# Optimization experiments

Measured on AMD Instinct MI355X. Metric: run time of the kernel, lower is better.

Reference implementation:

```python
import jax, jax.numpy as jnp
import numpy as np

N_REC = 12288  # 12 * nside^2, nside=32


def _mlp(x, w1, b1, w2, b2):
    # two-layer MLP with SiLU, as in GraphCast-style edge embedders
    return jnp.dot(jax.nn.silu(jnp.dot(x, w1) + b1), w2) + b2


def setup_inputs() -> dict:
    key = jax.random.key(0)
    ks = jax.random.split(key, 12)
    B, E, D_X, D_EDGE = 2, 393216, 128, 4
    EDGE_IN, EDGE_OUT, LIN_OUT = D_EDGE + D_X, 256, 256

    def glorot(k, shape):
        fan = shape[0] + shape[1]
        return jax.random.normal(k, shape, jnp.float32) * jnp.sqrt(2.0 / fan)

    return {
        "x": jax.random.normal(ks[0], (B, E, D_X), jnp.float32),
        "edge_attr": jax.random.normal(ks[1], (E, D_EDGE), jnp.float32),
        "edge_index": jax.random.randint(ks[2], (2, E), 0, N_REC, jnp.int64),
        "w1e": glorot(ks[3], (EDGE_IN, EDGE_OUT)),
        "b1e": jnp.zeros((EDGE_OUT,), jnp.float32),
        "w2e": glorot(ks[4], (EDGE_OUT, EDGE_OUT)),
        "b2e": jnp.zeros((EDGE_OUT,), jnp.float32),
        "w1f": glorot(ks[5], (EDGE_OUT, LIN_OUT)),
        "b1f": jnp.zeros((LIN_OUT,), jnp.float32),
        "w2f": glorot(ks[6], (LIN_OUT, LIN_OUT)),
        "b2f": jnp.zeros((LIN_OUT,), jnp.float32),
    }


def reference(x, edge_attr, edge_index, w1e, b1e, w2e, b2e, w1f, b1f, w2f, b2f):
    B = x.shape[0]
    # broadcast edge_attr over batch and concat with per-edge grid features
    ea = jnp.broadcast_to(edge_attr[None], (B,) + edge_attr.shape)  # [B,E,d_edge]
    v_g_prime = jnp.concatenate([ea, x], axis=-1)                    # [B,E,edge_in]
    v_g = _mlp(v_g_prime, w1e, b1e, w2e, b2e)                        # [B,E,edge_out]
    # scatter-sum edges into receiver nodes (edge_index[1]) along dim 1
    recv = edge_index[1]
    v_m_sum = jnp.zeros((B, N_REC, v_g.shape[-1]), v_g.dtype).at[:, recv].add(v_g)
    return _mlp(v_m_sum, w1f, b1f, w2f, b2f)                         # [B,N_REC,lin_out]
```

## Files before the change

### kernel.cpp

```cpp
#include <hip/hip_runtime.h>
#include <hip/hip_bf16.h>

#define E_EDGES 393216
#define NRECV   12288
#define DX      128
#define BATCH   2

typedef short bf16x8 __attribute__((ext_vector_type(8)));
typedef float f32x4  __attribute__((ext_vector_type(4)));

__device__ __forceinline__ unsigned short f2bf(float f) {
  union { float f; unsigned u; } v; v.f = f;
  unsigned r = v.u + 0x7FFFu + ((v.u >> 16) & 1u);
  return (unsigned short)(r >> 16);
}

__device__ __forceinline__ unsigned pk2(float a, float b) {
  __hip_bfloat162 h = __float22bfloat162_rn(make_float2(a, b));
  union { __hip_bfloat162 h; unsigned u; } c; c.h = h;
  return c.u;
}

__device__ __forceinline__ float silu_f(float v) {
  float e = __builtin_amdgcn_exp2f(v * -1.44269504089f);
  return v * __builtin_amdgcn_rcpf(1.0f + e);
}

__global__ __launch_bounds__(256) void zero_kernel(float4* __restrict__ p, int n4) {
  int i = blockIdx.x * 256 + threadIdx.x;
  int stride = gridDim.x * 256;
  float4 z = make_float4(0.f, 0.f, 0.f, 0.f);
  for (; i < n4; i += stride) p[i] = z;
}

__global__ __launch_bounds__(256) void swz_all_kernel(
    const float* __restrict__ w1e, const float* __restrict__ b1e,
    const float* __restrict__ w2e, const float* __restrict__ w1f,
    const float* __restrict__ w2f,
    unsigned short* __restrict__ w1sw, unsigned short* __restrict__ w2esw,
    unsigned short* __restrict__ w1fsw, unsigned short* __restrict__ w2fsw) {
  int blk = blockIdx.x;
  if (blk < 160) {
    int t = blk * 256 + threadIdx.x;
    int j = t & 7, l = (t >> 3) & 63, rest = t >> 9;
    int nf = rest & 15, ks = rest >> 4;
    int k = ks * 32 + (l >> 4) * 8 + j;
    int n = nf * 16 + (l & 15);
    float v = (k < 132) ? w1e[k * 256 + n] : (k == 132 ? b1e[n] : 0.0f);
    w1sw[t] = f2bf(v);
  } else {
    int g = blk - 160;
    int which = g >> 8;
    int t = (g & 255) * 256 + threadIdx.x;
    const float* W = (which == 0) ? w2e : (which == 1) ? w1f : w2f;
    unsigned short* O = (which == 0) ? w2esw : (which == 1) ? w1fsw : w2fsw;
    int j = t & 7, l = (t >> 3) & 63, rest = t >> 9;
    int nf = rest & 15, ks = rest >> 4;
    int k = ks * 32 + (l >> 4) * 8 + j;
    int n = nf * 16 + (l & 15);
    O[t] = f2bf(W[k * 256 + n]);
  }
}

__global__ void hist_kernel(const int* __restrict__ recv, int* __restrict__ cnt) {
  int e = blockIdx.x * 256 + threadIdx.x;
  if (e < E_EDGES) atomicAdd(&cnt[recv[e]], 1);
}

__global__ __launch_bounds__(256) void scan_kernel(const int* __restrict__ cnt,
                                                   int* __restrict__ head) {
  __shared__ int ts[256];
  const int t = threadIdx.x;
  const int base = t * 48;
  int s = 0;
#pragma unroll
  for (int i = 0; i < 48; ++i) s += cnt[base + i];
  ts[t] = s;
  __syncthreads();
  for (int d = 1; d < 256; d <<= 1) {
    int v = (t >= d) ? ts[t - d] : 0;
    __syncthreads();
    ts[t] += v;
    __syncthreads();
  }
  int run = (t == 0) ? 0 : ts[t - 1];
  for (int i = 0; i < 48; ++i) { head[base + i] = run; run += cnt[base + i]; }
}

__global__ void scatter_kernel(const int* __restrict__ recv, int* __restrict__ head,
                               int* __restrict__ perm) {
  int e = blockIdx.x * 256 + threadIdx.x;
  if (e < E_EDGES) {
    int pos = atomicAdd(&head[recv[e]], 1);
    perm[pos] = e;
  }
}

__global__ __launch_bounds__(256, 4) void edge_kernel(
    const float* __restrict__ x, const float* __restrict__ edge_attr,
    const int* __restrict__ recv, const int* __restrict__ perm,
    const unsigned short* __restrict__ w1sw, float* __restrict__ s) {
  __shared__ __align__(16) char As[64 * 384];
  __shared__ int rs[64];
  __shared__ int seg_recv[64];
  __shared__ unsigned seg32[16];

  const int tid = threadIdx.x;
  const int l  = tid & 63;
  const int w  = tid >> 6;
  const int lo = l & 15, hi = l >> 4;
  const int p0 = blockIdx.x * 64;
  const int b  = blockIdx.y;

  const int r = tid >> 2, q = tid & 3;
  const int er = perm[p0 + r];
  const float4* xr = (const float4*)(x + ((size_t)b * E_EDGES + er) * DX);
  float4 xv[8];
#pragma unroll
  for (int i = 0; i < 8; ++i) xv[i] = xr[i * 4 + q];

  float4 ea;
  if (tid < 64) {
    int e1 = perm[p0 + tid];
    rs[tid] = recv[e1];
    ea = *(const float4*)(edge_attr + (size_t)e1 * 4);
  }

  for (int idx = tid; idx < 960; idx += 256) {
    int rr = idx / 15, k2 = idx - rr * 15;
    int byte0 = 264 + 8 * k2;
    uint2 vz = make_uint2(k2 == 0 ? 0x00003F80u : 0u, 0u);
    *(uint2*)(As + rr * 384 + (byte0 ^ ((rr & 7) << 4))) = vz;
  }

  {
    const int rx = (r & 7) << 4;
#pragma unroll
    for (int i = 0; i < 8; ++i) {
      int t = i * 4 + q;
      int byte0 = 8 + 8 * t;
      *(uint2*)(As + r * 384 + (byte0 ^ rx)) =
          make_uint2(pk2(xv[i].x, xv[i].y), pk2(xv[i].z, xv[i].w));
    }
  }
  if (tid < 64) {
    *(uint2*)(As + tid * 384 + ((tid & 7) << 4)) =
        make_uint2(pk2(ea.x, ea.y), pk2(ea.z, ea.w));
  }
  __syncthreads();

  const int flag = (l == 63) || (rs[l + 1] != rs[l]);
  const unsigned long long segmask = __ballot(flag);
  const int nseg = __popcll(segmask);
  if (tid < 64) {
    int sid = __popcll(segmask & ((1ull << tid) - 1ull));
    ((unsigned char*)seg32)[tid] = (unsigned char)sid;
    if (flag) seg_recv[sid] = rs[tid];
  }

  f32x4 acc[4][4] = {};
  const int axor = (lo & 7) << 4;
  const unsigned short* wbase = w1sw + ((size_t)(w * 4) * 64 + l) * 8;
  bf16x8 cur0 = *(const bf16x8*)(wbase + 0 * 512);
  bf16x8 cur1 = *(const bf16x8*)(wbase + 1 * 512);
  bf16x8 cur2 = *(const bf16x8*)(wbase + 2 * 512);
  bf16x8 cur3 = *(const bf16x8*)(wbase + 3 * 512);
#pragma unroll
  for (int kk = 0; kk < 5; ++kk) {
    bf16x8 a[4];
#pragma unroll
    for (int mf = 0; mf < 4; ++mf)
      a[mf] = *(const bf16x8*)(As + (mf * 16 + lo) * 384 + ((kk * 64 + hi * 16) ^ axor));
    bf16x8 nxt0, nxt1, nxt2, nxt3;
    if (kk < 4) {
      const unsigned short* wn = wbase + (size_t)(kk + 1) * 8192;
      nxt0 = *(const bf16x8*)(wn + 0 * 512);
      nxt1 = *(const bf16x8*)(wn + 1 * 512);
      nxt2 = *(const bf16x8*)(wn + 2 * 512);
      nxt3 = *(const bf16x8*)(wn + 3 * 512);
    }
    __builtin_amdgcn_s_setprio(1);
#pragma unroll
    for (int mf = 0; mf < 4; ++mf)
      acc[mf][0] = __builtin_amdgcn_mfma_f32_16x16x32_bf16(a[mf], cur0, acc[mf][0], 0, 0, 0);
#pragma unroll
    for (int mf = 0; mf < 4; ++mf)
      acc[mf][1] = __builtin_amdgcn_mfma_f32_16x16x32_bf16(a[mf], cur1, acc[mf][1], 0, 0, 0);
#pragma unroll
    for (int mf = 0; mf < 4; ++mf)
      acc[mf][2] = __builtin_amdgcn_mfma_f32_16x16x32_bf16(a[mf], cur2, acc[mf][2], 0, 0, 0);
#pragma unroll
    for (int mf = 0; mf < 4; ++mf)
      acc[mf][3] = __builtin_amdgcn_mfma_f32_16x16x32_bf16(a[mf], cur3, acc[mf][3], 0, 0, 0);
    __builtin_amdgcn_s_setprio(0);
    if (kk < 4) { cur0 = nxt0; cur1 = nxt1; cur2 = nxt2; cur3 = nxt3; }
  }
  __syncthreads();

  unsigned pkd[4][4][2];
#pragma unroll
  for (int mf = 0; mf < 4; ++mf)
#pragma unroll
    for (int nf = 0; nf < 4; ++nf) {
      float v0 = silu_f(acc[mf][nf][0]);
      float v1 = silu_f(acc[mf][nf][1]);
      float v2 = silu_f(acc[mf][nf][2]);
      float v3 = silu_f(acc[mf][nf][3]);
      pkd[mf][nf][0] = pk2(v0, v1);
      pkd[mf][nf][1] = pk2(v2, v3);
    }

  unsigned hbw[2][4][4];
#pragma unroll
  for (int kk = 0; kk < 2; ++kk)
#pragma unroll
    for (int nf = 0; nf < 4; ++nf)
#pragma unroll
      for (int t = 0; t < 4; ++t) {
        int src = ((hi & 1) * 2 + (t >> 1)) * 16 + lo;
        int a0 = __shfl((int)pkd[2 * kk][nf][t & 1], src, 64);
        int a1 = __shfl((int)pkd[2 * kk + 1][nf][t & 1], src, 64);
        hbw[kk][nf][t] = (hi & 2) ? (unsigned)a1 : (unsigned)a0;
      }

  float* sb = s + (size_t)b * NRECV * 256;
  for (int p = 0; p * 16 < nseg; ++p) {
    union { unsigned u[4]; bf16x8 v; } ia[2];
#pragma unroll
    for (int kk = 0; kk < 2; ++kk) {
      unsigned d0 = seg32[kk * 8 + hi * 2];
      unsigned d1 = seg32[kk * 8 + hi * 2 + 1];
      unsigned tgt = (unsigned)(lo + p * 16);
      ia[kk].u[0] = (((d0 & 255u) == tgt) ? 0x3F80u : 0u) |
                    ((((d0 >> 8) & 255u) == tgt) ? 0x3F800000u : 0u);
      ia[kk].u[1] = ((((d0 >> 16) & 255u) == tgt) ? 0x3F80u : 0u) |
                    (((d0 >> 24) == tgt) ? 0x3F800000u : 0u);
      ia[kk].u[2] = (((d1 & 255u) == tgt) ? 0x3F80u : 0u) |
                    ((((d1 >> 8) & 255u) == tgt) ? 0x3F800000u : 0u);
      ia[kk].u[3] = ((((d1 >> 16) & 255u) == tgt) ? 0x3F80u : 0u) |
                    (((d1 >> 24) == tgt) ? 0x3F800000u : 0u);
    }
    f32x4 accS[4] = {};
    __builtin_amdgcn_s_setprio(1);
#pragma unroll
    for (int kk = 0; kk < 2; ++kk)
#pragma unroll
      for (int nf = 0; nf < 4; ++nf) {
        union { unsigned u[4]; bf16x8 v; } hb;
        hb.u[0] = hbw[kk][nf][0]; hb.u[1] = hbw[kk][nf][1];
        hb.u[2] = hbw[kk][nf][2]; hb.u[3] = hbw[kk][nf][3];
        accS[nf] = __builtin_amdgcn_mfma_f32_16x16x32_bf16(ia[kk].v, hb.v, accS[nf], 0, 0, 0);
      }
    __builtin_amdgcn_s_setprio(0);
#pragma unroll
    for (int j = 0; j < 4; ++j) {
      int sidx = p * 16 + hi * 4 + j;
      if (sidx < nseg) {
        int rcv = seg_recv[sidx];
#pragma unroll
        for (int nf = 0; nf < 4; ++nf)
          atomicAdd(sb + (size_t)rcv * 256 + w * 64 + nf * 16 + lo, accS[nf][j]);
      }
    }
  }
}

__device__ __forceinline__ void gemm64(const unsigned short* Ns,
                                       const unsigned short* __restrict__ Bsw,
                                       int w, int l, f32x4 acc[4][4]) {
  const int lo = l & 15, hi = l >> 4;
#pragma unroll
  for (int kk = 0; kk < 8; ++kk) {
    bf16x8 a[4], bb[4];
#pragma unroll
    for (int mf = 0; mf < 4; ++mf)
      a[mf] = *(const bf16x8*)&Ns[(mf * 16 + lo) * 264 + kk * 32 + hi * 8];
#pragma unroll
    for (int nf = 0; nf < 4; ++nf)
      bb[nf] = *(const bf16x8*)&Bsw[(size_t)(((kk * 16) + (w * 4 + nf)) * 64 + l) * 8];
#pragma unroll
    for (int mf = 0; mf < 4; ++mf)
#pragma unroll
      for (int nf = 0; nf < 4; ++nf)
        acc[mf][nf] = __builtin_amdgcn_mfma_f32_16x16x32_bf16(a[mf], bb[nf], acc[mf][nf], 0, 0, 0);
  }
}

__global__ __launch_bounds__(256) void node_kernel(
    const float* __restrict__ s, const int* __restrict__ cnt,
    const unsigned short* __restrict__ w2esw, const float* __restrict__ b2e,
    const unsigned short* __restrict__ w1fsw, const float* __restrict__ b1f,
    const unsigned short* __restrict__ w2fsw, const float* __restrict__ b2f,
    float* __restrict__ out) {
  __shared__ unsigned short Ns[64 * 264];
  __shared__ int   cntl[64];
  __shared__ float bias1[256], bias2[256], bias3[256];

  const int tid = threadIdx.x;
  const int l  = tid & 63;
  const int w  = tid >> 6;
  const int lo = l & 15, hi = l >> 4;
  const int r0 = blockIdx.x * 64;
  const int b  = blockIdx.y;

  const float4* sb = (const float4*)(s + ((size_t)b * NRECV + r0) * 256);
#pragma unroll
  for (int i = 0; i < 16; ++i) {
    int f = i * 256 + tid;
    float4 v = sb[f];
    int g = f * 4;
    int row = g >> 8, col = g & 255;
    *(uint2*)&Ns[row * 264 + col] = make_uint2(pk2(v.x, v.y), pk2(v.z, v.w));
  }
  if (tid < 64) cntl[tid] = cnt[r0 + tid];
  bias1[tid] = b2e[tid];
  bias2[tid] = b1f[tid];
  bias3[tid] = b2f[tid];
  __syncthreads();

  {
    f32x4 acc[4][4] = {};
    gemm64(Ns, w2esw, w, l, acc);
    __syncthreads();
#pragma unroll
    for (int mf = 0; mf < 4; ++mf)
#pragma unroll
      for (int nf = 0; nf < 4; ++nf) {
        const int col = w * 64 + nf * 16 + lo;
#pragma unroll
        for (int j = 0; j < 4; ++j) {
          const int row = mf * 16 + hi * 4 + j;
          float v = acc[mf][nf][j] + (float)cntl[row] * bias1[col];
          Ns[row * 264 + col] = f2bf(v);
        }
      }
    __syncthreads();
  }
  {
    f32x4 acc[4][4] = {};
    gemm64(Ns, w1fsw, w, l, acc);
    __syncthreads();
#pragma unroll
    for (int mf = 0; mf < 4; ++mf)
#pragma unroll
      for (int nf = 0; nf < 4; ++nf) {
        const int col = w * 64 + nf * 16 + lo;
#pragma unroll
        for (int j = 0; j < 4; ++j) {
          const int row = mf * 16 + hi * 4 + j;
          float v = silu_f(acc[mf][nf][j] + bias2[col]);
          Ns[row * 264 + col] = f2bf(v);
        }
      }
    __syncthreads();
  }
  {
    f32x4 acc[4][4] = {};
    gemm64(Ns, w2fsw, w, l, acc);
#pragma unroll
    for (int mf = 0; mf < 4; ++mf)
#pragma unroll
      for (int nf = 0; nf < 4; ++nf) {
        const int col = w * 64 + nf * 16 + lo;
#pragma unroll
        for (int j = 0; j < 4; ++j) {
          const int row = mf * 16 + hi * 4 + j;
          out[((size_t)b * NRECV + r0 + row) * 256 + col] = acc[mf][nf][j] + bias3[col];
        }
      }
  }
}

extern "C" void kernel_launch(void* const* d_in, const int* in_sizes, int n_in,
                              void* d_out, int out_size, void* d_ws, size_t ws_size,
                              hipStream_t stream) {
  const float* x         = (const float*)d_in[0];
  const float* edge_attr = (const float*)d_in[1];
  const int*   edge_idx  = (const int*)d_in[2];
  const float* w1e       = (const float*)d_in[3];
  const float* b1e       = (const float*)d_in[4];
  const float* w2e       = (const float*)d_in[5];
  const float* b2e       = (const float*)d_in[6];
  const float* w1f       = (const float*)d_in[7];
  const float* b1f       = (const float*)d_in[8];
  const float* w2f       = (const float*)d_in[9];
  const float* b2f       = (const float*)d_in[10];
  float* out = (float*)d_out;

  char* ws = (char*)d_ws;
  float*          sbuf  = (float*)(ws + 0);
  int*            cnt   = (int*)(ws + 25165824);
  int*            head  = (int*)(ws + 25214976);
  int*            perm  = (int*)(ws + 25264128);
  unsigned short* w1sw  = (unsigned short*)(ws + 26836992);
  unsigned short* w2esw = (unsigned short*)(ws + 26918912);
  unsigned short* w1fsw = (unsigned short*)(ws + 27049984);
  unsigned short* w2fsw = (unsigned short*)(ws + 27181056);

  zero_kernel<<<2048, 256, 0, stream>>>((float4*)ws, 1575936);

  swz_all_kernel<<<928, 256, 0, stream>>>(w1e, b1e, w2e, w1f, w2f,
                                          w1sw, w2esw, w1fsw, w2fsw);

  const int* recv = edge_idx + E_EDGES;
  hist_kernel<<<E_EDGES / 256, 256, 0, stream>>>(recv, cnt);
  scan_kernel<<<1, 256, 0, stream>>>(cnt, head);
  scatter_kernel<<<E_EDGES / 256, 256, 0, stream>>>(recv, head, perm);

  dim3 eg(E_EDGES / 64, BATCH);
  edge_kernel<<<eg, 256, 0, stream>>>(x, edge_attr, recv, perm, w1sw, sbuf);

  dim3 ng(NRECV / 64, BATCH);
  node_kernel<<<ng, 256, 0, stream>>>(sbuf, cnt, w2esw, b2e, w1fsw, b1f, w2fsw, b2f, out);
}
```

Baseline: 243.0 us.

## Process both batches per edge block, prefetching batch-1 features during batch-0 compute

The edge kernel now handles both batch elements in one block instead of launching a second grid dimension. The perm, recv, segment metadata and edge_attr setup is done once and reused for both batches. Batch-1 x rows are loaded into registers while batch-0's SiLU and scatter run, hiding that load latency. Block indices are also remapped with an interleave of stride 768, which changes the order in which blocks walk the edge range. In exchange the block does twice the work serially, with fewer blocks overall and higher register pressure from the prefetched rows.

```diff
diff --git a/kernel.cpp b/kernel.cpp
--- a/kernel.cpp
+++ b/kernel.cpp
@@ -109,20 +109,21 @@
   const int l  = tid & 63;
   const int w  = tid >> 6;
   const int lo = l & 15, hi = l >> 4;
-  const int p0 = blockIdx.x * 64;
-  const int b  = blockIdx.y;
+  const int bid = blockIdx.x;
+  const int p0 = ((bid & 7) * 768 + (bid >> 3)) * 64;
 
   const int r = tid >> 2, q = tid & 3;
   const int er = perm[p0 + r];
-  const float4* xr = (const float4*)(x + ((size_t)b * E_EDGES + er) * DX);
+  const float4* xr = (const float4*)(x + (size_t)er * DX);
   float4 xv[8];
 #pragma unroll
   for (int i = 0; i < 8; ++i) xv[i] = xr[i * 4 + q];
 
   float4 ea;
+  int rsv = 0;
   if (tid < 64) {
     int e1 = perm[p0 + tid];
-    rs[tid] = recv[e1];
+    rsv = recv[e1];
     ea = *(const float4*)(edge_attr + (size_t)e1 * 4);
   }
 
@@ -133,19 +134,18 @@
     *(uint2*)(As + rr * 384 + (byte0 ^ ((rr & 7) << 4))) = vz;
   }
 
-  {
-    const int rx = (r & 7) << 4;
-#pragma unroll
-    for (int i = 0; i < 8; ++i) {
-      int t = i * 4 + q;
-      int byte0 = 8 + 8 * t;
-      *(uint2*)(As + r * 384 + (byte0 ^ rx)) =
-          make_uint2(pk2(xv[i].x, xv[i].y), pk2(xv[i].z, xv[i].w));
-    }
+  const int rx = (r & 7) << 4;
+#pragma unroll
+  for (int i = 0; i < 8; ++i) {
+    int t = i * 4 + q;
+    int byte0 = 8 + 8 * t;
+    *(uint2*)(As + r * 384 + (byte0 ^ rx)) =
+        make_uint2(pk2(xv[i].x, xv[i].y), pk2(xv[i].z, xv[i].w));
   }
   if (tid < 64) {
     *(uint2*)(As + tid * 384 + ((tid & 7) << 4)) =
         make_uint2(pk2(ea.x, ea.y), pk2(ea.z, ea.w));
+    rs[tid] = rsv;
   }
   __syncthreads();
 
@@ -155,7 +155,7 @@
   if (tid < 64) {
     int sid = __popcll(segmask & ((1ull << tid) - 1ull));
     ((unsigned char*)seg32)[tid] = (unsigned char)sid;
-    if (flag) seg_recv[sid] = rs[tid];
+    if (flag) seg_recv[sid] = rsv;
   }
 
   f32x4 acc[4][4] = {};
@@ -197,17 +197,19 @@
   }
   __syncthreads();
 
+  __builtin_amdgcn_sched_barrier(0);
+  const float4* yr = (const float4*)(x + ((size_t)E_EDGES + er) * DX);
+  float4 y[8];
+#pragma unroll
+  for (int i = 0; i < 8; ++i) y[i] = yr[i * 4 + q];
+
   unsigned pkd[4][4][2];
 #pragma unroll
   for (int mf = 0; mf < 4; ++mf)
 #pragma unroll
     for (int nf = 0; nf < 4; ++nf) {
-      float v0 = silu_f(acc[mf][nf][0]);
-      float v1 = silu_f(acc[mf][nf][1]);
-      float v2 = silu_f(acc[mf][nf][2]);
-      float v3 = silu_f(acc[mf][nf][3]);
-      pkd[mf][nf][0] = pk2(v0, v1);
-      pkd[mf][nf][1] = pk2(v2, v3);
+      pkd[mf][nf][0] = pk2(silu_f(acc[mf][nf][0]), silu_f(acc[mf][nf][1]));
+      pkd[mf][nf][1] = pk2(silu_f(acc[mf][nf][2]), silu_f(acc[mf][nf][3]));
     }
 
   unsigned hbw[2][4][4];
@@ -223,7 +225,6 @@
         hbw[kk][nf][t] = (hi & 2) ? (unsigned)a1 : (unsigned)a0;
       }
 
-  float* sb = s + (size_t)b * NRECV * 256;
   for (int p = 0; p * 16 < nseg; ++p) {
     union { unsigned u[4]; bf16x8 v; } ia[2];
 #pragma unroll
@@ -259,7 +260,114 @@
         int rcv = seg_recv[sidx];
 #pragma unroll
         for (int nf = 0; nf < 4; ++nf)
-          atomicAdd(sb + (size_t)rcv * 256 + w * 64 + nf * 16 + lo, accS[nf][j]);
+          atomicAdd(s + (size_t)rcv * 256 + w * 64 + nf * 16 + lo, accS[nf][j]);
+      }
+    }
+  }
+
+#pragma unroll
+  for (int i = 0; i < 8; ++i) {
+    int t = i * 4 + q;
+    int byte0 = 8 + 8 * t;
+    *(uint2*)(As + r * 384 + (byte0 ^ rx)) =
+        make_uint2(pk2(y[i].x, y[i].y), pk2(y[i].z, y[i].w));
+  }
+  __syncthreads();
+
+#pragma unroll
+  for (int mf = 0; mf < 4; ++mf)
+#pragma unroll
+    for (int nf = 0; nf < 4; ++nf) acc[mf][nf] = (f32x4){0.f, 0.f, 0.f, 0.f};
+  cur0 = *(const bf16x8*)(wbase + 0 * 512);
+  cur1 = *(const bf16x8*)(wbase + 1 * 512);
+  cur2 = *(const bf16x8*)(wbase + 2 * 512);
+  cur3 = *(const bf16x8*)(wbase + 3 * 512);
+#pragma unroll
+  for (int kk = 0; kk < 5; ++kk) {
+    bf16x8 a[4];
+#pragma unroll
+    for (int mf = 0; mf < 4; ++mf)
+      a[mf] = *(const bf16x8*)(As + (mf * 16 + lo) * 384 + ((kk * 64 + hi * 16) ^ axor));
+    bf16x8 nxt0, nxt1, nxt2, nxt3;
+    if (kk < 4) {
+      const unsigned short* wn = wbase + (size_t)(kk + 1) * 8192;
+      nxt0 = *(const bf16x8*)(wn + 0 * 512);
+      nxt1 = *(const bf16x8*)(wn + 1 * 512);
+      nxt2 = *(const bf16x8*)(wn + 2 * 512);
+      nxt3 = *(const bf16x8*)(wn + 3 * 512);
+    }
+    __builtin_amdgcn_s_setprio(1);
+#pragma unroll
+    for (int mf = 0; mf < 4; ++mf)
+      acc[mf][0] = __builtin_amdgcn_mfma_f32_16x16x32_bf16(a[mf], cur0, acc[mf][0], 0, 0, 0);
+#pragma unroll
+    for (int mf = 0; mf < 4; ++mf)
+      acc[mf][1] = __builtin_amdgcn_mfma_f32_16x16x32_bf16(a[mf], cur1, acc[mf][1], 0, 0, 0);
+#pragma unroll
+    for (int mf = 0; mf < 4; ++mf)
+      acc[mf][2] = __builtin_amdgcn_mfma_f32_16x16x32_bf16(a[mf], cur2, acc[mf][2], 0, 0, 0);
+#pragma unroll
+    for (int mf = 0; mf < 4; ++mf)
+      acc[mf][3] = __builtin_amdgcn_mfma_f32_16x16x32_bf16(a[mf], cur3, acc[mf][3], 0, 0, 0);
+    __builtin_amdgcn_s_setprio(0);
+    if (kk < 4) { cur0 = nxt0; cur1 = nxt1; cur2 = nxt2; cur3 = nxt3; }
+  }
+
+#pragma unroll
+  for (int mf = 0; mf < 4; ++mf)
+#pragma unroll
+    for (int nf = 0; nf < 4; ++nf) {
+      pkd[mf][nf][0] = pk2(silu_f(acc[mf][nf][0]), silu_f(acc[mf][nf][1]));
+      pkd[mf][nf][1] = pk2(silu_f(acc[mf][nf][2]), silu_f(acc[mf][nf][3]));
+    }
+#pragma unroll
+  for (int kk = 0; kk < 2; ++kk)
+#pragma unroll
+    for (int nf = 0; nf < 4; ++nf)
+#pragma unroll
+      for (int t = 0; t < 4; ++t) {
+        int src = ((hi & 1) * 2 + (t >> 1)) * 16 + lo;
+        int a0 = __shfl((int)pkd[2 * kk][nf][t & 1], src, 64);
+        int a1 = __shfl((int)pkd[2 * kk + 1][nf][t & 1], src, 64);
+        hbw[kk][nf][t] = (hi & 2) ? (unsigned)a1 : (unsigned)a0;
+      }
+  float* s1 = s + (size_t)NRECV * 256;
+  for (int p = 0; p * 16 < nseg; ++p) {
+    union { unsigned u[4]; bf16x8 v; } ia[2];
+#pragma unroll
+    for (int kk = 0; kk < 2; ++kk) {
+      unsigned d0 = seg32[kk * 8 + hi * 2];
+      unsigned d1 = seg32[kk * 8 + hi * 2 + 1];
+      unsigned tgt = (unsigned)(lo + p * 16);
+      ia[kk].u[0] = (((d0 & 255u) == tgt) ? 0x3F80u : 0u) |
+                    ((((d0 >> 8) & 255u) == tgt) ? 0x3F800000u : 0u);
+      ia[kk].u[1] = ((((d0 >> 16) & 255u) == tgt) ? 0x3F80u : 0u) |
+                    (((d0 >> 24) == tgt) ? 0x3F800000u : 0u);
+      ia[kk].u[2] = (((d1 & 255u) == tgt) ? 0x3F80u : 0u) |
+                    ((((d1 >> 8) & 255u) == tgt) ? 0x3F800000u : 0u);
+      ia[kk].u[3] = ((((d1 >> 16) & 255u) == tgt) ? 0x3F80u : 0u) |
+                    (((d1 >> 24) == tgt) ? 0x3F800000u : 0u);
+    }
+    f32x4 accS[4] = {};
+    __builtin_amdgcn_s_setprio(1);
+#pragma unroll
+    for (int kk = 0; kk < 2; ++kk)
+#pragma unroll
+      for (int nf = 0; nf < 4; ++nf) {
+        union { unsigned u[4]; bf16x8 v; } hb;
+        hb.u[0] = hbw[kk][nf][0]; hb.u[1] = hbw[kk][nf][1];
+        hb.u[2] = hbw[kk][nf][2]; hb.u[3] = hbw[kk][nf][3];
+        accS[nf] = __builtin_amdgcn_mfma_f32_16x16x32_bf16(ia[kk].v, hb.v, accS[nf], 0, 0, 0);
+      }
+    __builtin_amdgcn_s_setprio(0);
+#pragma unroll
+    for (int j = 0; j < 4; ++j) {
+      int sidx = p * 16 + hi * 4 + j;
+      if (sidx < nseg) {
+        int rcv = seg_recv[sidx];
+#pragma unroll
+        for (int nf = 0; nf < 4; ++nf)
+          atomicAdd(s1 + (size_t)rcv * 256 + w * 64 + nf * 16 + lo, accS[nf][j]);
       }
     }
   }
@@ -407,8 +515,7 @@
   scan_kernel<<<1, 256, 0, stream>>>(cnt, head);
   scatter_kernel<<<E_EDGES / 256, 256, 0, stream>>>(recv, head, perm);
 
-  dim3 eg(E_EDGES / 64, BATCH);
-  edge_kernel<<<eg, 256, 0, stream>>>(x, edge_attr, recv, perm, w1sw, sbuf);
+  edge_kernel<<<E_EDGES / 64, 256, 0, stream>>>(x, edge_attr, recv, perm, w1sw, sbuf);
 
   dim3 ng(NRECV / 64, BATCH);
   node_kernel<<<ng, 256, 0, stream>>>(sbuf, cnt, w2esw, b2e, w1fsw, b1f, w2fsw, b2f, out);
```

After: 325.7 us. 34.0% more time.
